# Kernel tuning notes

Hardware: AMD Instinct MI355X
Metric: run time of the kernel (lower is better)

## Reference

```python
import jax, jax.numpy as jnp
import numpy as np

V = 50257   # vocab size
E = 256     # embedding_dimension
D = 8       # key_query_reduced_dimensionality
H = 8       # no_of_attention_heads
L = 16      # no_of_blocks
B = 8       # batch
T = 512     # seq len == context_size
FF = 4 * E  # MLP hidden


def setup_inputs() -> dict:
    key = jax.random.key(0)
    ks = jax.random.split(key, 12)
    rn = lambda k, s: jax.random.normal(k, s, jnp.float32) * 0.02
    return {
        'tokens': jax.random.randint(ks[0], (B, T), 0, V),
        'ideal_value': jax.random.randint(ks[1], (B, T), 0, V),
        'tok_emb': rn(ks[2], (V, E)),
        'pos_emb': rn(ks[3], (T, E)),
        'Wq': rn(ks[4], (L, H, E, D)),
        'Wk': rn(ks[5], (L, H, E, D)),
        'Wv': rn(ks[6], (L, H, E, D)),
        'Wo': rn(ks[7], (L, H * D, E)),
        'bo': jnp.zeros((L, E), jnp.float32),
        'ln1_s': jnp.ones((L, E), jnp.float32),
        'ln1_b': jnp.zeros((L, E), jnp.float32),
        'W1': rn(ks[8], (L, E, FF)),
        'b1': jnp.zeros((L, FF), jnp.float32),
        'W2': rn(ks[9], (L, FF, E)),
        'b2': jnp.zeros((L, E), jnp.float32),
        'ln2_s': jnp.ones((L, E), jnp.float32),
        'ln2_b': jnp.zeros((L, E), jnp.float32),
        'lnf_s': jnp.ones((E,), jnp.float32),
        'lnf_b': jnp.zeros((E,), jnp.float32),
        'Wf': rn(ks[10], (E, V)),
        'bf': jnp.zeros((V,), jnp.float32),
    }


def _ln(x, s, b):
    m = x.mean(-1, keepdims=True)
    v = ((x - m) ** 2).mean(-1, keepdims=True)
    return (x - m) * jax.lax.rsqrt(v + 1e-5) * s + b


def reference(tokens, ideal_value, tok_emb, pos_emb, Wq, Wk, Wv, Wo, bo,
              ln1_s, ln1_b, W1, b1, W2, b2, ln2_s, ln2_b, lnf_s, lnf_b, Wf, bf):
    Bn, Tn = tokens.shape
    x = tok_emb[tokens] + pos_emb[:Tn]                      # [B,T,E]
    # faithful mask: masked_fill where transpose(tril(R))==0 -> keep upper triangle
    keep = jnp.triu(jnp.ones((D, D), bool))
    scale = jnp.float32(E) ** 0.5

    def block(x, p):
        wq, wk, wv, wo, bo_, s1, bb1, w1, bm1, w2, bm2, s2, bb2 = p
        h = _ln(x, s1, bb1)
        Q = jnp.einsum('bte,hed->bhtd', h, wq)              # [B,H,T,D]
        K = jnp.einsum('bte,hed->bhtd', h, wk)
        Vv = jnp.einsum('bte,hed->bhtd', h, wv)
        # R = K^T @ Q : feature-by-feature [B,H,D,D] (this repo's quirky attention)
        R = jnp.einsum('bhti,bhtj->bhij', K, Q) / scale
        R = jax.nn.softmax(jnp.where(keep, R, -jnp.inf), axis=-1)
        a = jnp.einsum('bhti,bhij->bhtj', Vv, R)            # V @ R, [B,H,T,D]
        a = a.transpose(0, 2, 1, 3).reshape(x.shape[0], x.shape[1], H * D)
        x = x + a @ wo + bo_                                # dropout is identity (eval)
        h2 = _ln(x, s2, bb2)
        x = x + jax.nn.relu(h2 @ w1 + bm1) @ w2 + bm2
        return x, None

    x, _ = jax.lax.scan(block, x, (Wq, Wk, Wv, Wo, bo, ln1_s, ln1_b,
                                   W1, b1, W2, b2, ln2_s, ln2_b))
    logits = (_ln(x, lnf_s, lnf_b) @ Wf + bf).reshape(-1, V)  # [B*T, V]
    tgt = ideal_value.reshape(-1)
    logp = jax.nn.log_softmax(logits, axis=-1)
    loss = -jnp.take_along_axis(logp, tgt[:, None], axis=1).mean()
    return logits, loss
```

## Files before the change

kernel.cpp:

```cpp
#include <hip/hip_runtime.h>
#include <math.h>

#define V_SZ 50257
#define NPAD 50432
#define NCB 197

#define AS1 __attribute__((address_space(1)))
#define AS3 __attribute__((address_space(3)))

typedef short s16x8 __attribute__((ext_vector_type(8)));
typedef ushort u16x4 __attribute__((ext_vector_type(4)));
typedef float f32x4 __attribute__((ext_vector_type(4)));

__device__ __forceinline__ ushort f2bf(float x) {
    union { float f; unsigned u; } v; v.f = x;
    unsigned r = v.u + 0x7FFF + ((v.u >> 16) & 1);
    return (ushort)(r >> 16);
}
__device__ __forceinline__ float bf2f(ushort u) {
    union { unsigned u; float f; } v; v.u = ((unsigned)u) << 16; return v.f;
}

__global__ __launch_bounds__(256) void gpt_embed_ln(const int* __restrict__ tokens,
                                                    const float* __restrict__ tok_emb,
                                                    const float* __restrict__ pos_emb,
                                                    const float* __restrict__ s, const float* __restrict__ b,
                                                    float* __restrict__ x, ushort* __restrict__ hb) {
    int wave = threadIdx.x >> 6, lane = threadIdx.x & 63;
    int row = blockIdx.x * 4 + wave;
    int t = row & 511;
    int tok = tokens[row];
    float4 te = ((const float4*)(tok_emb + tok * 256))[lane];
    float4 pe = ((const float4*)(pos_emb + t * 256))[lane];
    float4 v = make_float4(te.x + pe.x, te.y + pe.y, te.z + pe.z, te.w + pe.w);
    ((float4*)(x + row * 256))[lane] = v;
    float sum = v.x + v.y + v.z + v.w;
    #pragma unroll
    for (int off = 1; off < 64; off <<= 1) sum += __shfl_xor(sum, off);
    float mean = sum * (1.0f / 256.0f);
    float dx = v.x - mean, dy = v.y - mean, dz = v.z - mean, dw = v.w - mean;
    float vs = dx * dx + dy * dy + dz * dz + dw * dw;
    #pragma unroll
    for (int off = 1; off < 64; off <<= 1) vs += __shfl_xor(vs, off);
    float rstd = rsqrtf(vs * (1.0f / 256.0f) + 1e-5f);
    float4 sv = ((const float4*)s)[lane];
    float4 bv = ((const float4*)b)[lane];
    u16x4 o;
    o[0] = f2bf(dx * rstd * sv.x + bv.x);
    o[1] = f2bf(dy * rstd * sv.y + bv.y);
    o[2] = f2bf(dz * rstd * sv.z + bv.z);
    o[3] = f2bf(dw * rstd * sv.w + bv.w);
    *(u16x4*)&hb[row * 256 + lane * 4] = o;
}

__global__ __launch_bounds__(256) void cvt_transpose(const float* __restrict__ in, ushort* __restrict__ out,
                                                     int Kd, int Nd, int n_real,
                                                     int in_stride, int out_stride) {
    __shared__ __align__(16) ushort t[64][80];
    const float* inp = in + (size_t)blockIdx.z * in_stride;
    ushort* outp = out + (size_t)blockIdx.z * out_stride;
    int n0 = blockIdx.x * 64, k0 = blockIdx.y * 64;
    int tid = threadIdx.x;
    #pragma unroll
    for (int p = 0; p < 4; p++) {
        int lk = p * 16 + (tid >> 4);
        int ln = (tid & 15) * 4;
        int k = k0 + lk, n = n0 + ln;
        const float* rowp = inp + (size_t)k * Nd;
        float v0 = 0.f, v1 = 0.f, v2 = 0.f, v3 = 0.f;
        if (n + 0 < n_real) v0 = rowp[n + 0];
        if (n + 1 < n_real) v1 = rowp[n + 1];
        if (n + 2 < n_real) v2 = rowp[n + 2];
        if (n + 3 < n_real) v3 = rowp[n + 3];
        t[ln + 0][lk] = f2bf(v0);
        t[ln + 1][lk] = f2bf(v1);
        t[ln + 2][lk] = f2bf(v2);
        t[ln + 3][lk] = f2bf(v3);
    }
    __syncthreads();
    int ln = tid >> 2, kq = (tid & 3) * 16;
    ushort* op = outp + (size_t)(n0 + ln) * Kd + k0 + kq;
    *(s16x8*)&op[0] = *(const s16x8*)&t[ln][kq];
    *(s16x8*)&op[8] = *(const s16x8*)&t[ln][kq + 8];
}

__global__ __launch_bounds__(256) void cvt_qkv(const float* __restrict__ Wq, const float* __restrict__ Wk,
                                               const float* __restrict__ Wv, ushort* __restrict__ WqkvT) {
    int l = blockIdx.x, kind = blockIdx.y;
    const float* W = (kind == 0 ? Wq : (kind == 1 ? Wk : Wv)) + l * 16384;
    ushort* out = WqkvT + (size_t)l * 65536 + kind * 64 * 256;
    int tid = threadIdx.x;
    #pragma unroll 4
    for (int it = 0; it < 64; it++) {
        int idx = it * 256 + tid;
        int row = idx >> 8, e = idx & 255;
        int h = row >> 3, d = row & 7;
        out[row * 256 + e] = f2bf(W[h * 2048 + e * 8 + d]);
    }
    if (kind == 0) {
        ushort* zp = WqkvT + (size_t)l * 65536 + 192 * 256;
        #pragma unroll 4
        for (int it = 0; it < 64; it++) zp[it * 256 + tid] = 0;
    }
}

__global__ __launch_bounds__(512, 4) void gpt_pre(const ushort* __restrict__ hb,
                                                  const ushort* __restrict__ WqkvT,
                                                  ushort* __restrict__ Vb,
                                                  float* __restrict__ Rpart) {
    __shared__ __align__(16) ushort As[16 * 64];
    __shared__ __align__(16) ushort Bs[256 * 64];
    __shared__ float kqv[16][193];
    const int tid = threadIdx.x, lane = tid & 63, wn = tid >> 6;
    const int rows0 = blockIdx.x * 16;
    const int fr = lane & 15, fkb = (lane >> 4) * 16;
    const int arow = tid >> 3, ach = tid & 7;

    f32x4 acc[2];
    acc[0] = (f32x4)0.0f; acc[1] = (f32x4)0.0f;

    s16x8 ra, rb[4];
    if (tid < 128) ra = *(const s16x8*)&hb[(size_t)(rows0 + arow) * 256 + ach * 8];
    #pragma unroll
    for (int i = 0; i < 4; i++) {
        int u = tid + i * 512, r = u >> 3, ch = u & 7;
        rb[i] = *(const s16x8*)&WqkvT[(size_t)r * 256 + ch * 8];
    }
    #pragma unroll 1
    for (int kt = 0; kt < 4; kt++) {
        if (kt) __syncthreads();
        if (tid < 128)
            *(s16x8*)&As[arow * 64 + (((ach * 16) ^ ((arow & 7) << 4)) >> 1)] = ra;
        #pragma unroll
        for (int i = 0; i < 4; i++) {
            int u = tid + i * 512, r = u >> 3, ch = u & 7;
            *(s16x8*)&Bs[r * 64 + (((ch * 16) ^ ((r & 7) << 4)) >> 1)] = rb[i];
        }
        __syncthreads();
        if (kt < 3) {
            int k0 = (kt + 1) * 64;
            if (tid < 128) ra = *(const s16x8*)&hb[(size_t)(rows0 + arow) * 256 + k0 + ach * 8];
            #pragma unroll
            for (int i = 0; i < 4; i++) {
                int u = tid + i * 512, r = u >> 3, ch = u & 7;
                rb[i] = *(const s16x8*)&WqkvT[(size_t)r * 256 + k0 + ch * 8];
            }
        }
        #pragma unroll
        for (int kk = 0; kk < 2; kk++) {
            int kbyte = kk * 64 + fkb;
            s16x8 af = *(const s16x8*)&As[fr * 64 + ((kbyte ^ ((fr & 7) << 4)) >> 1)];
            #pragma unroll
            for (int n = 0; n < 2; n++) {
                int brow = wn * 32 + n * 16 + fr;
                s16x8 bfv = *(const s16x8*)&Bs[brow * 64 + ((kbyte ^ ((brow & 7) << 4)) >> 1)];
                acc[n] = __builtin_amdgcn_mfma_f32_16x16x32_bf16(af, bfv, acc[n], 0, 0, 0);
            }
        }
    }
    #pragma unroll
    for (int n = 0; n < 2; n++) {
        int col = wn * 32 + n * 16 + fr;
        if (col < 192) {
            #pragma unroll
            for (int r = 0; r < 4; r++)
                kqv[(lane >> 4) * 4 + r][col] = acc[n][r];
        }
    }
    __syncthreads();
    #pragma unroll
    for (int i = 0; i < 2; i++) {
        int u = tid + i * 512, t = u >> 6, hd = u & 63;
        Vb[(size_t)(rows0 + t) * 64 + hd] = f2bf(kqv[t][128 + hd]);
    }
    {
        int h = tid >> 6, i2 = (tid >> 3) & 7, j = tid & 7;
        float s = 0.0f;
        #pragma unroll
        for (int t = 0; t < 16; t++)
            s += kqv[t][64 + h * 8 + i2] * kqv[t][h * 8 + j];
        int bb = rows0 >> 9, part = (rows0 >> 4) & 31;
        Rpart[(size_t)(bb * 32 + part) * 512 + tid] = s;
    }
}

__global__ __launch_bounds__(512, 4) void gpt_layer(
        const float* __restrict__ Rpart_in, const ushort* __restrict__ Vb_in,
        const ushort* __restrict__ WoT, const float* __restrict__ bo,
        const ushort* __restrict__ W1T, const float* __restrict__ b1,
        const ushort* __restrict__ W2T, const float* __restrict__ b2,
        const float* __restrict__ ls2, const float* __restrict__ lb2,
        const float* __restrict__ nls, const float* __restrict__ nlb,
        float* __restrict__ x,
        const ushort* __restrict__ WqkvT_next,
        ushort* __restrict__ Vb_out, float* __restrict__ Rpart_out,
        ushort* __restrict__ hbout, int mode) {
    __shared__ __align__(16) ushort Bs[256 * 64];
    __shared__ __align__(16) ushort ffs[16 * 1024];
    __shared__ __align__(16) ushort h2s[16 * 256];
    __shared__ __align__(16) ushort abl[16 * 64];
    __shared__ __align__(16) ushort Vl[16 * 64];
    __shared__ float Rs[512];
    __shared__ float red1[16][8], red2[16][8], mrow[16], rrow[16];

    const int tid = threadIdx.x, lane = tid & 63, wn = tid >> 6;
    const int rows0 = blockIdx.x * 16, b = rows0 >> 9;
    const int fr = lane & 15, fkb = (lane >> 4) * 16, rbase = (lane >> 4) * 4;
    int colv[2]; colv[0] = wn * 32 + fr; colv[1] = wn * 32 + 16 + fr;

    {
        const float* rp = Rpart_in + (size_t)b * 32 * 512 + tid;
        float s = 0.0f;
        #pragma unroll
        for (int p = 0; p < 32; p++) s += rp[p * 512];
        s *= (1.0f / 16.0f);
        int ii = (tid >> 3) & 7, j = tid & 7;
        float val = (j >= ii) ? s : -INFINITY;
        float m = val;
        #pragma unroll
        for (int off = 1; off < 8; off <<= 1) m = fmaxf(m, __shfl_xor(m, off, 8));
        float ex = __expf(val - m);
        float su = ex;
        #pragma unroll
        for (int off = 1; off < 8; off <<= 1) su += __shfl_xor(su, off, 8);
        Rs[tid] = ex / su;
    }
    #pragma unroll
    for (int i = 0; i < 2; i++) {
        int u = tid + i * 512, t = u >> 6, hd = u & 63;
        Vl[t * 64 + hd] = Vb_in[(size_t)(rows0 + t) * 64 + hd];
    }
    __syncthreads();
    #pragma unroll
    for (int i = 0; i < 2; i++) {
        int u = tid + i * 512, t = u >> 6, hd = u & 63, h = hd >> 3, j = hd & 7;
        float a = 0.0f;
        #pragma unroll
        for (int q = 0; q < 8; q++)
            a += bf2f(Vl[t * 64 + h * 8 + q]) * Rs[h * 64 + q * 8 + j];
        abl[t * 64 + (((hd * 2) ^ ((t & 7) << 4)) >> 1)] = f2bf(a);
    }
    s16x8 rbv[4];
    #pragma unroll
    for (int i = 0; i < 4; i++) {
        int u = tid + i * 512, r = u >> 3, ch = u & 7;
        rbv[i] = *(const s16x8*)&WoT[(size_t)r * 64 + ch * 8];
    }
    __syncthreads();
    #pragma unroll
    for (int i = 0; i < 4; i++) {
        int u = tid + i * 512, r = u >> 3, ch = u & 7;
        *(s16x8*)&Bs[r * 64 + (((ch * 16) ^ ((r & 7) << 4)) >> 1)] = rbv[i];
    }
    __syncthreads();
    f32x4 acc[2];
    acc[0] = (f32x4)0.0f; acc[1] = (f32x4)0.0f;
    #pragma unroll
    for (int kk = 0; kk < 2; kk++) {
        int kbyte = kk * 64 + fkb;
        s16x8 af = *(const s16x8*)&abl[fr * 64 + ((kbyte ^ ((fr & 7) << 4)) >> 1)];
        #pragma unroll
        for (int n = 0; n < 2; n++) {
            int brow = wn * 32 + n * 16 + fr;
            s16x8 bfv = *(const s16x8*)&Bs[brow * 64 + ((kbyte ^ ((brow & 7) << 4)) >> 1)];
            acc[n] = __builtin_amdgcn_mfma_f32_16x16x32_bf16(af, bfv, acc[n], 0, 0, 0);
        }
    }
    float xn[2][4];
    #pragma unroll
    for (int n = 0; n < 2; n++) {
        int col = colv[n];
        float bbv = bo[col];
        #pragma unroll
        for (int r = 0; r < 4; r++)
            xn[n][r] = acc[n][r] + bbv + x[(size_t)(rows0 + rbase + r) * 256 + col];
    }
    #pragma unroll
    for (int r = 0; r < 4; r++) {
        float s1 = xn[0][r] + xn[1][r];
        float s2 = xn[0][r] * xn[0][r] + xn[1][r] * xn[1][r];
        #pragma unroll
        for (int off = 1; off < 16; off <<= 1) {
            s1 += __shfl_xor(s1, off);
            s2 += __shfl_xor(s2, off);
        }
        if (fr == 0) { red1[rbase + r][wn] = s1; red2[rbase + r][wn] = s2; }
    }
    __syncthreads();
    if (tid < 16) {
        float s1 = 0.f, s2 = 0.f;
        #pragma unroll
        for (int w = 0; w < 8; w++) { s1 += red1[tid][w]; s2 += red2[tid][w]; }
        float mean = s1 * (1.0f / 256.0f);
        float var = s2 * (1.0f / 256.0f) - mean * mean;
        mrow[tid] = mean;
        rrow[tid] = rsqrtf(var + 1e-5f);
    }
    __syncthreads();
    #pragma unroll
    for (int n = 0; n < 2; n++) {
        int col = colv[n];
        float lsv = ls2[col], lbv = lb2[col];
        #pragma unroll
        for (int r = 0; r < 4; r++) {
            int rl = rbase + r;
            float hv = (xn[n][r] - mrow[rl]) * rrow[rl] * lsv + lbv;
            h2s[rl * 256 + (((col * 2) ^ ((rl & 7) << 4)) >> 1)] = f2bf(hv);
        }
    }
    #pragma unroll 1
    for (int c = 0; c < 4; c++) {
        const ushort* Bg = W1T + (size_t)c * 256 * 256;
        acc[0] = (f32x4)0.0f; acc[1] = (f32x4)0.0f;
        #pragma unroll
        for (int i = 0; i < 4; i++) {
            int u = tid + i * 512, r = u >> 3, ch = u & 7;
            rbv[i] = *(const s16x8*)&Bg[(size_t)r * 256 + ch * 8];
        }
        #pragma unroll 1
        for (int kt = 0; kt < 4; kt++) {
            __syncthreads();
            #pragma unroll
            for (int i = 0; i < 4; i++) {
                int u = tid + i * 512, r = u >> 3, ch = u & 7;
                *(s16x8*)&Bs[r * 64 + (((ch * 16) ^ ((r & 7) << 4)) >> 1)] = rbv[i];
            }
            __syncthreads();
            if (kt < 3) {
                int k0 = (kt + 1) * 64;
                #pragma unroll
                for (int i = 0; i < 4; i++) {
                    int u = tid + i * 512, r = u >> 3, ch = u & 7;
                    rbv[i] = *(const s16x8*)&Bg[(size_t)r * 256 + k0 + ch * 8];
                }
            }
            #pragma unroll
            for (int kk = 0; kk < 2; kk++) {
                int kbyte = kt * 128 + kk * 64 + fkb;
                s16x8 af = *(const s16x8*)&h2s[fr * 256 + ((kbyte ^ ((fr & 7) << 4)) >> 1)];
                int kb2 = kk * 64 + fkb;
                #pragma unroll
                for (int n = 0; n < 2; n++) {
                    int brow = wn * 32 + n * 16 + fr;
                    s16x8 bfv = *(const s16x8*)&Bs[brow * 64 + ((kb2 ^ ((brow & 7) << 4)) >> 1)];
                    acc[n] = __builtin_amdgcn_mfma_f32_16x16x32_bf16(af, bfv, acc[n], 0, 0, 0);
                }
            }
        }
        #pragma unroll
        for (int n = 0; n < 2; n++) {
            int col = c * 256 + colv[n];
            float bb1 = b1[col];
            #pragma unroll
            for (int r = 0; r < 4; r++) {
                int rl = rbase + r;
                ffs[rl * 1024 + (((col * 2) ^ ((rl & 7) << 4)) >> 1)] =
                    f2bf(fmaxf(acc[n][r] + bb1, 0.0f));
            }
        }
    }
    f32x4 a2[2];
    a2[0] = (f32x4)0.0f; a2[1] = (f32x4)0.0f;
    #pragma unroll
    for (int i = 0; i < 4; i++) {
        int u = tid + i * 512, r = u >> 3, ch = u & 7;
        rbv[i] = *(const s16x8*)&W2T[(size_t)r * 1024 + ch * 8];
    }
    #pragma unroll 1
    for (int kt = 0; kt < 16; kt++) {
        __syncthreads();
        #pragma unroll
        for (int i = 0; i < 4; i++) {
            int u = tid + i * 512, r = u >> 3, ch = u & 7;
            *(s16x8*)&Bs[r * 64 + (((ch * 16) ^ ((r & 7) << 4)) >> 1)] = rbv[i];
        }
        __syncthreads();
        if (kt < 15) {
            int k0 = (kt + 1) * 64;
            #pragma unroll
            for (int i = 0; i < 4; i++) {
                int u = tid + i * 512, r = u >> 3, ch = u & 7;
                rbv[i] = *(const s16x8*)&W2T[(size_t)r * 1024 + k0 + ch * 8];
            }
        }
        #pragma unroll
        for (int kk = 0; kk < 2; kk++) {
            int kbyte = kt * 128 + kk * 64 + fkb;
            s16x8 af = *(const s16x8*)&ffs[fr * 1024 + ((kbyte ^ ((fr & 7) << 4)) >> 1)];
            int kb2 = kk * 64 + fkb;
            #pragma unroll
            for (int n = 0; n < 2; n++) {
                int brow = wn * 32 + n * 16 + fr;
                s16x8 bfv = *(const s16x8*)&Bs[brow * 64 + ((kb2 ^ ((brow & 7) << 4)) >> 1)];
                a2[n] = __builtin_amdgcn_mfma_f32_16x16x32_bf16(af, bfv, a2[n], 0, 0, 0);
            }
        }
    }
    #pragma unroll
    for (int n = 0; n < 2; n++) {
        int col = colv[n];
        float bb2 = b2[col];
        #pragma unroll
        for (int r = 0; r < 4; r++) {
            float v = xn[n][r] + a2[n][r] + bb2;
            xn[n][r] = v;
            x[(size_t)(rows0 + rbase + r) * 256 + col] = v;
        }
    }
    __syncthreads();
    #pragma unroll
    for (int r = 0; r < 4; r++) {
        float s1 = xn[0][r] + xn[1][r];
        float s2 = xn[0][r] * xn[0][r] + xn[1][r] * xn[1][r];
        #pragma unroll
        for (int off = 1; off < 16; off <<= 1) {
            s1 += __shfl_xor(s1, off);
            s2 += __shfl_xor(s2, off);
        }
        if (fr == 0) { red1[rbase + r][wn] = s1; red2[rbase + r][wn] = s2; }
    }
    __syncthreads();
    if (tid < 16) {
        float s1 = 0.f, s2 = 0.f;
        #pragma unroll
        for (int w = 0; w < 8; w++) { s1 += red1[tid][w]; s2 += red2[tid][w]; }
        float mean = s1 * (1.0f / 256.0f);
        float var = s2 * (1.0f / 256.0f) - mean * mean;
        mrow[tid] = mean;
        rrow[tid] = rsqrtf(var + 1e-5f);
    }
    __syncthreads();
    #pragma unroll
    for (int n = 0; n < 2; n++) {
        int col = colv[n];
        float lsv = nls[col], lbv = nlb[col];
        #pragma unroll
        for (int r = 0; r < 4; r++) {
            int rl = rbase + r;
            float hv = (xn[n][r] - mrow[rl]) * rrow[rl] * lsv + lbv;
            ushort hu = f2bf(hv);
            h2s[rl * 256 + (((col * 2) ^ ((rl & 7) << 4)) >> 1)] = hu;
            if (mode == 0)
                hbout[(size_t)(rows0 + rl) * 256 + col] = hu;
        }
    }
    if (mode == 0) return;

    float* kqv = (float*)ffs;
    acc[0] = (f32x4)0.0f; acc[1] = (f32x4)0.0f;
    #pragma unroll
    for (int i = 0; i < 4; i++) {
        int u = tid + i * 512, r = u >> 3, ch = u & 7;
        rbv[i] = *(const s16x8*)&WqkvT_next[(size_t)r * 256 + ch * 8];
    }
    #pragma unroll 1
    for (int kt = 0; kt < 4; kt++) {
        __syncthreads();
        #pragma unroll
        for (int i = 0; i < 4; i++) {
            int u = tid + i * 512, r = u >> 3, ch = u & 7;
            *(s16x8*)&Bs[r * 64 + (((ch * 16) ^ ((r & 7) << 4)) >> 1)] = rbv[i];
        }
        __syncthreads();
        if (kt < 3) {
            int k0 = (kt + 1) * 64;
            #pragma unroll
            for (int i = 0; i < 4; i++) {
                int u = tid + i * 512, r = u >> 3, ch = u & 7;
                rbv[i] = *(const s16x8*)&WqkvT_next[(size_t)r * 256 + k0 + ch * 8];
            }
        }
        #pragma unroll
        for (int kk = 0; kk < 2; kk++) {
            int kbyte = kt * 128 + kk * 64 + fkb;
            s16x8 af = *(const s16x8*)&h2s[fr * 256 + ((kbyte ^ ((fr & 7) << 4)) >> 1)];
            int kb2 = kk * 64 + fkb;
            #pragma unroll
            for (int n = 0; n < 2; n++) {
                int brow = wn * 32 + n * 16 + fr;
                s16x8 bfv = *(const s16x8*)&Bs[brow * 64 + ((kb2 ^ ((brow & 7) << 4)) >> 1)];
                acc[n] = __builtin_amdgcn_mfma_f32_16x16x32_bf16(af, bfv, acc[n], 0, 0, 0);
            }
        }
    }
    __syncthreads();
    #pragma unroll
    for (int n = 0; n < 2; n++) {
        int col = wn * 32 + n * 16 + fr;
        if (col < 192) {
            #pragma unroll
            for (int r = 0; r < 4; r++)
                kqv[(rbase + r) * 193 + col] = acc[n][r];
        }
    }
    __syncthreads();
    #pragma unroll
    for (int i = 0; i < 2; i++) {
        int u = tid + i * 512, t = u >> 6, hd = u & 63;
        Vb_out[(size_t)(rows0 + t) * 64 + hd] = f2bf(kqv[t * 193 + 128 + hd]);
    }
    {
        int h = tid >> 6, i2 = (tid >> 3) & 7, j = tid & 7;
        float s = 0.0f;
        #pragma unroll
        for (int t = 0; t < 16; t++)
            s += kqv[t * 193 + 64 + h * 8 + i2] * kqv[t * 193 + h * 8 + j];
        int part = (rows0 >> 4) & 31;
        Rpart_out[(size_t)(b * 32 + part) * 512 + tid] = s;
    }
}

__global__ __launch_bounds__(512, 4) void gpt_logits_mfma(const ushort* __restrict__ hb, const ushort* __restrict__ WfT,
                                                          const float* __restrict__ bfb, float* __restrict__ out,
                                                          float2* __restrict__ lsebuf) {
    __shared__ __align__(16) ushort As[128 * 64];
    __shared__ __align__(16) ushort Bs[256 * 64];
    f32x4 acc[4][4];
    int flat = blockIdx.y * 32 + blockIdx.x;
    int nf = (flat & 7) * 788 + (flat >> 3);
    int rb = nf & 31, cb = nf >> 5;
    int row0 = rb * 128, c0 = cb * 256;
    const int tid = threadIdx.x, lane = tid & 63, wid = tid >> 6;
    const int wm = wid >> 2, wn = wid & 3;
    const int fr = lane & 15, fkb = (lane >> 4) * 16;

    #pragma unroll
    for (int m = 0; m < 4; m++)
        #pragma unroll
        for (int n = 0; n < 4; n++) acc[m][n] = (f32x4)0.0f;

    const int srow = lane >> 3;
    const int sch = lane & 7;
    #pragma unroll 1
    for (int kt = 0; kt < 4; kt++) {
        if (kt) __syncthreads();
        {
            int kb = kt * 64;
            #pragma unroll
            for (int i = 0; i < 2; i++) {
                int rloc = wid * 16 + i * 8 + srow;
                int cs = sch ^ (rloc & 7);
                const ushort* gp = &hb[(size_t)(row0 + rloc) * 256 + kb + cs * 8];
                __builtin_amdgcn_global_load_lds((const AS1 void*)gp,
                                                 (AS3 void*)&As[(wid * 16 + i * 8) * 64], 16, 0, 0);
            }
            #pragma unroll
            for (int i = 0; i < 4; i++) {
                int rloc = wid * 32 + i * 8 + srow;
                int cs = sch ^ (rloc & 7);
                const ushort* gp = &WfT[(size_t)(c0 + rloc) * 256 + kb + cs * 8];
                __builtin_amdgcn_global_load_lds((const AS1 void*)gp,
                                                 (AS3 void*)&Bs[(wid * 32 + i * 8) * 64], 16, 0, 0);
            }
        }
        __syncthreads();
        #pragma unroll
        for (int kk = 0; kk < 2; kk++) {
            int kbyte = kk * 64 + fkb;
            s16x8 af[4], bfr[4];
            #pragma unroll
            for (int m = 0; m < 4; m++) {
                int arow = wm * 64 + m * 16 + fr;
                af[m] = *(const s16x8*)&As[arow * 64 + ((kbyte ^ ((arow & 7) << 4)) >> 1)];
            }
            #pragma unroll
            for (int n = 0; n < 4; n++) {
                int brow = wn * 64 + n * 16 + fr;
                bfr[n] = *(const s16x8*)&Bs[brow * 64 + ((kbyte ^ ((brow & 7) << 4)) >> 1)];
            }
            #pragma unroll
            for (int m = 0; m < 4; m++)
                #pragma unroll
                for (int n = 0; n < 4; n++)
                    acc[m][n] = __builtin_amdgcn_mfma_f32_16x16x32_bf16(af[m], bfr[n], acc[m][n], 0, 0, 0);
        }
    }
    float bb[4]; int gcv[4];
    #pragma unroll
    for (int n = 0; n < 4; n++) {
        int gc = c0 + wn * 64 + n * 16 + fr;
        gcv[n] = gc;
        bb[n] = (gc < V_SZ) ? bfb[gc] : 0.0f;
    }
    __syncthreads();
    float2 (*red)[4] = (float2(*)[4])As;
    #pragma unroll
    for (int m = 0; m < 4; m++) {
        int rloc = wm * 64 + m * 16 + (lane >> 4) * 4;
        int gr = row0 + rloc;
        #pragma unroll
        for (int r = 0; r < 4; r++) {
            float v[4];
            float vmax = -1e30f;
            #pragma unroll
            for (int n = 0; n < 4; n++) {
                v[n] = (gcv[n] < V_SZ) ? acc[m][n][r] + bb[n] : -1e30f;
                vmax = fmaxf(vmax, v[n]);
            }
            #pragma unroll
            for (int n = 0; n < 4; n++)
                if (gcv[n] < V_SZ)
                    out[(size_t)(gr + r) * V_SZ + gcv[n]] = v[n];
            #pragma unroll
            for (int off = 1; off < 16; off <<= 1)
                vmax = fmaxf(vmax, __shfl_xor(vmax, off));
            float vsum = __expf(v[0] - vmax) + __expf(v[1] - vmax)
                       + __expf(v[2] - vmax) + __expf(v[3] - vmax);
            #pragma unroll
            for (int off = 1; off < 16; off <<= 1)
                vsum += __shfl_xor(vsum, off);
            if ((lane & 15) == 0)
                red[rloc + r][wn] = make_float2(vmax, vsum);
        }
    }
    __syncthreads();
    if (tid < 128) {
        float M = -1e30f, S = 0.0f;
        #pragma unroll
        for (int w = 0; w < 4; w++) {
            float2 p = red[tid][w];
            float M2 = fmaxf(M, p.x);
            S = S * __expf(M - M2) + p.y * __expf(p.x - M2);
            M = M2;
        }
        lsebuf[(size_t)(row0 + tid) * NCB + cb] = make_float2(M, S);
    }
}

__global__ __launch_bounds__(256) void gpt_lse(const float2* __restrict__ lsebuf, const float* __restrict__ out,
                                               const int* __restrict__ tgt, float* __restrict__ partial) {
    int wave = threadIdx.x >> 6, lane = threadIdx.x & 63;
    int row = blockIdx.x * 4 + wave;
    float m = -INFINITY, s = 0.0f;
    for (int i = lane; i < NCB; i += 64) {
        float2 p = lsebuf[(size_t)row * NCB + i];
        float M = fmaxf(m, p.x);
        s = s * __expf(m - M) + p.y * __expf(p.x - M);
        m = M;
    }
    #pragma unroll
    for (int off = 1; off < 64; off <<= 1) {
        float m2 = __shfl_xor(m, off);
        float s2 = __shfl_xor(s, off);
        float M = fmaxf(m, m2);
        s = s * __expf(m - M) + s2 * __expf(m2 - M);
        m = M;
    }
    if (lane == 0)
        partial[row] = m + logf(s) - out[(size_t)row * V_SZ + tgt[row]];
}

__global__ void gpt_loss_reduce(const float* __restrict__ partial, float* __restrict__ out) {
    __shared__ float red[256];
    int tid = threadIdx.x;
    float s = 0.0f;
    for (int i = tid; i < 4096; i += 256) s += partial[i];
    red[tid] = s;
    __syncthreads();
    for (int off = 128; off > 0; off >>= 1) {
        if (tid < off) red[tid] += red[tid + off];
        __syncthreads();
    }
    if (tid == 0) out[0] = red[0] * (1.0f / 4096.0f);
}

__global__ void gpt_embed(const int* __restrict__ tokens, const float* __restrict__ tok_emb,
                          const float* __restrict__ pos_emb, float* __restrict__ x) {
    int idx = blockIdx.x * 256 + threadIdx.x;
    int bt = idx >> 8, e = idx & 255;
    int t = bt & 511;
    int tok = tokens[bt];
    x[idx] = tok_emb[tok * 256 + e] + pos_emb[t * 256 + e];
}

__global__ void gpt_ln(const float* __restrict__ x, const float* __restrict__ s,
                       const float* __restrict__ b, float* __restrict__ h) {
    __shared__ float red[256];
    int row = blockIdx.x, e = threadIdx.x;
    float v = x[row * 256 + e];
    red[e] = v;
    __syncthreads();
    for (int off = 128; off > 0; off >>= 1) {
        if (e < off) red[e] += red[e + off];
        __syncthreads();
    }
    float mean = red[0] * (1.0f / 256.0f);
    __syncthreads();
    float d = v - mean;
    red[e] = d * d;
    __syncthreads();
    for (int off = 128; off > 0; off >>= 1) {
        if (e < off) red[e] += red[e + off];
        __syncthreads();
    }
    float rstd = rsqrtf(red[0] * (1.0f / 256.0f) + 1e-5f);
    h[row * 256 + e] = d * rstd * s[e] + b[e];
}

__global__ void gpt_qkv(const float* __restrict__ h, const float* __restrict__ Wq,
                        const float* __restrict__ Wk, const float* __restrict__ Wv,
                        float* __restrict__ Q, float* __restrict__ K, float* __restrict__ Vv) {
    __shared__ float hs[8][256];
    int tid = threadIdx.x;
    int row0 = blockIdx.x * 8;
    #pragma unroll
    for (int r = 0; r < 8; r++) hs[r][tid] = h[(row0 + r) * 256 + tid];
    __syncthreads();
    if (tid < 192) {
        int kind = tid >> 6, o = tid & 63, hh = o >> 3, d = o & 7;
        const float* W = kind == 0 ? Wq : (kind == 1 ? Wk : Wv);
        const float* wp = W + hh * 2048 + d;
        float acc[8];
        #pragma unroll
        for (int r = 0; r < 8; r++) acc[r] = 0.0f;
        for (int e = 0; e < 256; e++) {
            float w = wp[e * 8];
            #pragma unroll
            for (int r = 0; r < 8; r++) acc[r] += hs[r][e] * w;
        }
        float* outp = kind == 0 ? Q : (kind == 1 ? K : Vv);
        int b = row0 >> 9;
        #pragma unroll
        for (int r = 0; r < 8; r++) {
            int t = (row0 + r) & 511;
            outp[((b * 8 + hh) * 512 + t) * 8 + d] = acc[r];
        }
    }
}

__global__ void gpt_attn_r(const float* __restrict__ K, const float* __restrict__ Q,
                           float* __restrict__ R) {
    __shared__ __align__(16) float Ks[64][8];
    __shared__ __align__(16) float Qs[64][8];
    int bh = blockIdx.x, tid = threadIdx.x;
    int i = tid >> 3, j = tid & 7;
    const float* Kb = K + bh * 512 * 8;
    const float* Qb = Q + bh * 512 * 8;
    float acc = 0.0f;
    for (int t0 = 0; t0 < 512; t0 += 64) {
        *(float4*)&Ks[tid][0] = *(const float4*)&Kb[(t0 + tid) * 8];
        *(float4*)&Ks[tid][4] = *(const float4*)&Kb[(t0 + tid) * 8 + 4];
        *(float4*)&Qs[tid][0] = *(const float4*)&Qb[(t0 + tid) * 8];
        *(float4*)&Qs[tid][4] = *(const float4*)&Qb[(t0 + tid) * 8 + 4];
        __syncthreads();
        #pragma unroll 16
        for (int t = 0; t < 64; t++) acc += Ks[t][i] * Qs[t][j];
        __syncthreads();
    }
    acc *= (1.0f / 16.0f);
    float val = (j >= i) ? acc : -INFINITY;
    float m = val;
    #pragma unroll
    for (int off = 1; off < 8; off <<= 1) m = fmaxf(m, __shfl_xor(m, off, 8));
    float ex = expf(val - m);
    float sum = ex;
    #pragma unroll
    for (int off = 1; off < 8; off <<= 1) sum += __shfl_xor(sum, off, 8);
    R[bh * 64 + tid] = ex / sum;
}

__global__ void gpt_attn_out(const float* __restrict__ Vv, const float* __restrict__ R,
                             const float* __restrict__ Wo, const float* __restrict__ bo,
                             float* __restrict__ x) {
    __shared__ __align__(16) float as[8][64];
    int tid = threadIdx.x;
    int row0 = blockIdx.x * 8;
    int b = row0 >> 9;
    #pragma unroll
    for (int k = 0; k < 2; k++) {
        int idx = k * 256 + tid;
        int r = idx >> 6, hd = idx & 63;
        int hh = hd >> 3, jj = hd & 7;
        int t = (row0 + r) & 511;
        const float* vp = Vv + ((b * 8 + hh) * 512 + t) * 8;
        const float* rp = R + (b * 8 + hh) * 64 + jj;
        float a = 0.0f;
        #pragma unroll
        for (int i = 0; i < 8; i++) a += vp[i] * rp[i * 8];
        as[r][hd] = a;
    }
    __syncthreads();
    float acc[8];
    float bb = bo[tid];
    #pragma unroll
    for (int r = 0; r < 8; r++) acc[r] = bb;
    for (int hd0 = 0; hd0 < 64; hd0 += 4) {
        float w0 = Wo[(hd0 + 0) * 256 + tid];
        float w1 = Wo[(hd0 + 1) * 256 + tid];
        float w2 = Wo[(hd0 + 2) * 256 + tid];
        float w3 = Wo[(hd0 + 3) * 256 + tid];
        #pragma unroll
        for (int r = 0; r < 8; r++) {
            float4 av = *(const float4*)&as[r][hd0];
            acc[r] += av.x * w0 + av.y * w1 + av.z * w2 + av.w * w3;
        }
    }
    #pragma unroll
    for (int r = 0; r < 8; r++) x[(row0 + r) * 256 + tid] += acc[r];
}

__global__ __launch_bounds__(256) void gpt_mlp(const float* __restrict__ h, const float* __restrict__ W1,
                         const float* __restrict__ b1, const float* __restrict__ W2,
                         const float* __restrict__ b2, float* __restrict__ x) {
    __shared__ __align__(16) float hs[8][256];
    __shared__ __align__(16) float ffs[8][1024];
    int tid = threadIdx.x;
    int row0 = blockIdx.x * 8;
    #pragma unroll
    for (int r = 0; r < 8; r++) hs[r][tid] = h[(row0 + r) * 256 + tid];
    __syncthreads();
    {
        float acc[4][8];
        #pragma unroll
        for (int k = 0; k < 4; k++) {
            float bb = b1[k * 256 + tid];
            #pragma unroll
            for (int r = 0; r < 8; r++) acc[k][r] = bb;
        }
        for (int e0 = 0; e0 < 256; e0 += 4) {
            float w[4][4];
            #pragma unroll
            for (int ee = 0; ee < 4; ee++)
                #pragma unroll
                for (int k = 0; k < 4; k++)
                    w[ee][k] = W1[(e0 + ee) * 1024 + k * 256 + tid];
            #pragma unroll
            for (int r = 0; r < 8; r++) {
                float4 hv = *(const float4*)&hs[r][e0];
                #pragma unroll
                for (int k = 0; k < 4; k++)
                    acc[k][r] += hv.x * w[0][k] + hv.y * w[1][k] + hv.z * w[2][k] + hv.w * w[3][k];
            }
        }
        #pragma unroll
        for (int k = 0; k < 4; k++)
            #pragma unroll
            for (int r = 0; r < 8; r++)
                ffs[r][k * 256 + tid] = fmaxf(acc[k][r], 0.0f);
    }
    __syncthreads();
    {
        float acc[8];
        float bb = b2[tid];
        #pragma unroll
        for (int r = 0; r < 8; r++) acc[r] = bb;
        for (int f0 = 0; f0 < 1024; f0 += 4) {
            float w0 = W2[(f0 + 0) * 256 + tid];
            float w1 = W2[(f0 + 1) * 256 + tid];
            float w2 = W2[(f0 + 2) * 256 + tid];
            float w3 = W2[(f0 + 3) * 256 + tid];
            #pragma unroll
            for (int r = 0; r < 8; r++) {
                float4 fv = *(const float4*)&ffs[r][f0];
                acc[r] += fv.x * w0 + fv.y * w1 + fv.z * w2 + fv.w * w3;
            }
        }
        #pragma unroll
        for (int r = 0; r < 8; r++) x[(row0 + r) * 256 + tid] += acc[r];
    }
}

__global__ __launch_bounds__(256) void gpt_logits(const float* __restrict__ hf, const float* __restrict__ Wf,
                            const float* __restrict__ bf, float* __restrict__ out) {
    __shared__ __align__(16) float hs[32][256];
    int tid = threadIdx.x;
    int row0 = blockIdx.y * 32;
    #pragma unroll
    for (int r = 0; r < 32; r++) hs[r][tid] = hf[(row0 + r) * 256 + tid];
    __syncthreads();
    int c0 = blockIdx.x * 512 + tid;
    int c1 = c0 + 256;
    int c0c = c0 < V_SZ ? c0 : V_SZ - 1;
    int c1c = c1 < V_SZ ? c1 : V_SZ - 1;
    float acc0[32], acc1[32];
    float b0 = bf[c0c], b1 = bf[c1c];
    #pragma unroll
    for (int r = 0; r < 32; r++) { acc0[r] = b0; acc1[r] = b1; }
    const float* p0 = Wf + c0c;
    const float* p1 = Wf + c1c;
    for (int e0 = 0; e0 < 256; e0 += 4) {
        float w00 = p0[(size_t)(e0 + 0) * V_SZ];
        float w01 = p0[(size_t)(e0 + 1) * V_SZ];
        float w02 = p0[(size_t)(e0 + 2) * V_SZ];
        float w03 = p0[(size_t)(e0 + 3) * V_SZ];
        float w10 = p1[(size_t)(e0 + 0) * V_SZ];
        float w11 = p1[(size_t)(e0 + 1) * V_SZ];
        float w12 = p1[(size_t)(e0 + 2) * V_SZ];
        float w13 = p1[(size_t)(e0 + 3) * V_SZ];
        #pragma unroll
        for (int r = 0; r < 32; r++) {
            float4 hv = *(const float4*)&hs[r][e0];
            acc0[r] += hv.x * w00 + hv.y * w01 + hv.z * w02 + hv.w * w03;
            acc1[r] += hv.x * w10 + hv.y * w11 + hv.z * w12 + hv.w * w13;
        }
    }
    if (c0 < V_SZ) {
        #pragma unroll
        for (int r = 0; r < 32; r++) out[(size_t)(row0 + r) * V_SZ + c0] = acc0[r];
    }
    if (c1 < V_SZ) {
        #pragma unroll
        for (int r = 0; r < 32; r++) out[(size_t)(row0 + r) * V_SZ + c1] = acc1[r];
    }
}

__global__ void gpt_loss(const float* __restrict__ logits, const int* __restrict__ tgt,
                         float* __restrict__ partial) {
    __shared__ float ms[256], ss[256];
    int row = blockIdx.x, tid = threadIdx.x;
    const float* lr = logits + (size_t)row * V_SZ;
    float m = -INFINITY, s = 0.0f;
    for (int c = tid; c < V_SZ; c += 256) {
        float v = lr[c];
        float nm = fmaxf(m, v);
        s = s * expf(m - nm) + expf(v - nm);
        m = nm;
    }
    ms[tid] = m; ss[tid] = s;
    __syncthreads();
    for (int off = 128; off > 0; off >>= 1) {
        if (tid < off) {
            float m2 = ms[tid + off], s2 = ss[tid + off];
            float M = fmaxf(ms[tid], m2);
            ss[tid] = ss[tid] * expf(ms[tid] - M) + s2 * expf(m2 - M);
            ms[tid] = M;
        }
        __syncthreads();
    }
    if (tid == 0) {
        float lse = ms[0] + logf(ss[0]);
        partial[row] = lse - lr[tgt[row]];
    }
}

extern "C" void kernel_launch(void* const* d_in, const int* in_sizes, int n_in,
                              void* d_out, int out_size, void* d_ws, size_t ws_size,
                              hipStream_t stream) {
    const int*   tokens  = (const int*)d_in[0];
    const int*   ideal   = (const int*)d_in[1];
    const float* tok_emb = (const float*)d_in[2];
    const float* pos_emb = (const float*)d_in[3];
    const float* Wq      = (const float*)d_in[4];
    const float* Wk      = (const float*)d_in[5];
    const float* Wv      = (const float*)d_in[6];
    const float* Wo      = (const float*)d_in[7];
    const float* bo      = (const float*)d_in[8];
    const float* ln1_s   = (const float*)d_in[9];
    const float* ln1_b   = (const float*)d_in[10];
    const float* W1      = (const float*)d_in[11];
    const float* b1      = (const float*)d_in[12];
    const float* W2      = (const float*)d_in[13];
    const float* b2      = (const float*)d_in[14];
    const float* ln2_s   = (const float*)d_in[15];
    const float* ln2_b   = (const float*)d_in[16];
    const float* lnf_s   = (const float*)d_in[17];
    const float* lnf_b   = (const float*)d_in[18];
    const float* Wf      = (const float*)d_in[19];
    const float* bf      = (const float*)d_in[20];
    float* out = (float*)d_out;

    size_t off = 0;
    char* wsc = (char*)d_ws;
    ushort* WfT   = (ushort*)(wsc + off); off += (size_t)NPAD * 256 * 2;
    ushort* W1T   = (ushort*)(wsc + off); off += (size_t)16 * 1024 * 256 * 2;
    ushort* W2T   = (ushort*)(wsc + off); off += (size_t)16 * 256 * 1024 * 2;
    ushort* WqkvT = (ushort*)(wsc + off); off += (size_t)16 * 256 * 256 * 2;
    ushort* WoT   = (ushort*)(wsc + off); off += (size_t)16 * 256 * 64 * 2;
    ushort* hb    = (ushort*)(wsc + off); off += (size_t)4096 * 256 * 2;
    ushort* Vb0   = (ushort*)(wsc + off); off += (size_t)4096 * 64 * 2;
    ushort* Vb1   = (ushort*)(wsc + off); off += (size_t)4096 * 64 * 2;
    float*  x     = (float*)(wsc + off);  off += (size_t)4096 * 256 * 4;
    float*  Rp0   = (float*)(wsc + off);  off += (size_t)8 * 32 * 512 * 4;
    float*  Rp1   = (float*)(wsc + off);  off += (size_t)8 * 32 * 512 * 4;
    float*  partial = (float*)(wsc + off); off += (size_t)4096 * 4;
    float2* lsebuf = (float2*)(wsc + off); off += (size_t)4096 * NCB * 8;
    bool big = ws_size >= off;

    if (big) {
        cvt_transpose<<<dim3(16, 4, 16), 256, 0, stream>>>(W1, W1T, 256, 1024, 1024, 262144, 262144);
        cvt_transpose<<<dim3(4, 16, 16), 256, 0, stream>>>(W2, W2T, 1024, 256, 256, 262144, 262144);
        cvt_transpose<<<dim3(4, 1, 16), 256, 0, stream>>>(Wo, WoT, 64, 256, 256, 16384, 16384);
        cvt_transpose<<<dim3(788, 4, 1), 256, 0, stream>>>(Wf, WfT, 256, V_SZ, V_SZ, 0, 0);
        cvt_qkv<<<dim3(16, 3), 256, 0, stream>>>(Wq, Wk, Wv, WqkvT);

        gpt_embed_ln<<<1024, 256, 0, stream>>>(tokens, tok_emb, pos_emb, ln1_s, ln1_b, x, hb);
        gpt_pre<<<256, 512, 0, stream>>>(hb, WqkvT, Vb0, Rp0);

        for (int l = 0; l < 16; l++) {
            const float* nls = (l < 15) ? ln1_s + (l + 1) * 256 : lnf_s;
            const float* nlb = (l < 15) ? ln1_b + (l + 1) * 256 : lnf_b;
            const float* Rin = (l & 1) ? Rp1 : Rp0;
            const ushort* Vin = (l & 1) ? Vb1 : Vb0;
            float* Rout = (l & 1) ? Rp0 : Rp1;
            ushort* Vout = (l & 1) ? Vb0 : Vb1;
            int mode = (l < 15) ? 1 : 0;
            const ushort* Wnext = WqkvT + (size_t)((l < 15) ? (l + 1) : 0) * 65536;
            gpt_layer<<<256, 512, 0, stream>>>(Rin, Vin,
                                               WoT + (size_t)l * 16384, bo + l * 256,
                                               W1T + (size_t)l * 262144, b1 + l * 1024,
                                               W2T + (size_t)l * 262144, b2 + l * 256,
                                               ln2_s + l * 256, ln2_b + l * 256,
                                               nls, nlb, x,
                                               Wnext, Vout, Rout, hb, mode);
        }

        gpt_logits_mfma<<<dim3(32, NCB), 512, 0, stream>>>(hb, WfT, bf, out, lsebuf);
        gpt_lse<<<1024, 256, 0, stream>>>(lsebuf, out, ideal, partial);
        gpt_loss_reduce<<<1, 256, 0, stream>>>(partial, out + (size_t)4096 * V_SZ);
    } else {
        float* fx  = (float*)d_ws;
        float* fh  = fx + 4096 * 256;
        float* fQ  = fh + 4096 * 256;
        float* fK  = fQ + 4096 * 64;
        float* fV  = fK + 4096 * 64;
        float* fR  = fV + 4096 * 64;
        float* fpart = fR + 64 * 64;
        gpt_embed<<<4096, 256, 0, stream>>>(tokens, tok_emb, pos_emb, fx);
        for (int l = 0; l < 16; l++) {
            gpt_ln<<<4096, 256, 0, stream>>>(fx, ln1_s + l * 256, ln1_b + l * 256, fh);
            gpt_qkv<<<512, 256, 0, stream>>>(fh, Wq + l * 16384, Wk + l * 16384, Wv + l * 16384, fQ, fK, fV);
            gpt_attn_r<<<64, 64, 0, stream>>>(fK, fQ, fR);
            gpt_attn_out<<<512, 256, 0, stream>>>(fV, fR, Wo + l * 16384, bo + l * 256, fx);
            gpt_ln<<<4096, 256, 0, stream>>>(fx, ln2_s + l * 256, ln2_b + l * 256, fh);
            gpt_mlp<<<512, 256, 0, stream>>>(fh, W1 + l * 262144, b1 + l * 1024, W2 + l * 262144, b2 + l * 256, fx);
        }
        gpt_ln<<<4096, 256, 0, stream>>>(fx, lnf_s, lnf_b, fh);
        dim3 lg(99, 128);
        gpt_logits<<<lg, 256, 0, stream>>>(fh, Wf, bf, out);
        gpt_loss<<<4096, 256, 0, stream>>>(out, ideal, fpart);
        gpt_loss_reduce<<<1, 256, 0, stream>>>(fpart, out + (size_t)4096 * V_SZ);
    }
}
```

Baseline: 1.005 ms.

## Make B-tile LDS staging wave-private to drop per-k-step block barriers

Each wave now stages into shared memory only the 32 weight rows it consumes in its MFMAs, instead of all 512 threads cooperatively filling the whole 256-row tile. Because no other wave reads those rows, the two __syncthreads around every k-step in the Wo, W1, W2 and next-layer QKV loops are removed. A single barrier is kept at each phase boundary so the shared activation buffers (h2s, ffs) are visible to all waves. This relies on in-order LDS access within a wave and adds a small unroll of the W2 loop; the trade is less overlap of load latency across waves at barriers in exchange for removing barrier stalls.

```diff
diff --git a/kernel.cpp b/kernel.cpp
--- a/kernel.cpp
+++ b/kernel.cpp
@@ -207,6 +207,13 @@
     const int rows0 = blockIdx.x * 16, b = rows0 >> 9;
     const int fr = lane & 15, fkb = (lane >> 4) * 16, rbase = (lane >> 4) * 4;
     int colv[2]; colv[0] = wn * 32 + fr; colv[1] = wn * 32 + 16 + fr;
+    int srow_[4], sch_[4];
+    #pragma unroll
+    for (int i = 0; i < 4; i++) {
+        int u = lane + i * 64;
+        srow_[i] = wn * 32 + (u >> 3);
+        sch_[i] = u & 7;
+    }
 
     {
         const float* rp = Rpart_in + (size_t)b * 32 * 512 + tid;
@@ -242,17 +249,12 @@
     }
     s16x8 rbv[4];
     #pragma unroll
-    for (int i = 0; i < 4; i++) {
-        int u = tid + i * 512, r = u >> 3, ch = u & 7;
-        rbv[i] = *(const s16x8*)&WoT[(size_t)r * 64 + ch * 8];
-    }
-    __syncthreads();
-    #pragma unroll
-    for (int i = 0; i < 4; i++) {
-        int u = tid + i * 512, r = u >> 3, ch = u & 7;
-        *(s16x8*)&Bs[r * 64 + (((ch * 16) ^ ((r & 7) << 4)) >> 1)] = rbv[i];
-    }
-    __syncthreads();
+    for (int i = 0; i < 4; i++)
+        rbv[i] = *(const s16x8*)&WoT[(size_t)srow_[i] * 64 + sch_[i] * 8];
+    __syncthreads();
+    #pragma unroll
+    for (int i = 0; i < 4; i++)
+        *(s16x8*)&Bs[srow_[i] * 64 + (((sch_[i] * 16) ^ ((srow_[i] & 7) << 4)) >> 1)] = rbv[i];
     f32x4 acc[2];
     acc[0] = (f32x4)0.0f; acc[1] = (f32x4)0.0f;
     #pragma unroll
@@ -308,31 +310,24 @@
             h2s[rl * 256 + (((col * 2) ^ ((rl & 7) << 4)) >> 1)] = f2bf(hv);
         }
     }
+    __syncthreads();
     #pragma unroll 1
     for (int c = 0; c < 4; c++) {
         const ushort* Bg = W1T + (size_t)c * 256 * 256;
         acc[0] = (f32x4)0.0f; acc[1] = (f32x4)0.0f;
         #pragma unroll
-        for (int i = 0; i < 4; i++) {
-            int u = tid + i * 512, r = u >> 3, ch = u & 7;
-            rbv[i] = *(const s16x8*)&Bg[(size_t)r * 256 + ch * 8];
-        }
+        for (int i = 0; i < 4; i++)
+            rbv[i] = *(const s16x8*)&Bg[(size_t)srow_[i] * 256 + sch_[i] * 8];
         #pragma unroll 1
         for (int kt = 0; kt < 4; kt++) {
-            __syncthreads();
-            #pragma unroll
-            for (int i = 0; i < 4; i++) {
-                int u = tid + i * 512, r = u >> 3, ch = u & 7;
-                *(s16x8*)&Bs[r * 64 + (((ch * 16) ^ ((r & 7) << 4)) >> 1)] = rbv[i];
-            }
-            __syncthreads();
+            #pragma unroll
+            for (int i = 0; i < 4; i++)
+                *(s16x8*)&Bs[srow_[i] * 64 + (((sch_[i] * 16) ^ ((srow_[i] & 7) << 4)) >> 1)] = rbv[i];
             if (kt < 3) {
                 int k0 = (kt + 1) * 64;
                 #pragma unroll
-                for (int i = 0; i < 4; i++) {
-                    int u = tid + i * 512, r = u >> 3, ch = u & 7;
-                    rbv[i] = *(const s16x8*)&Bg[(size_t)r * 256 + k0 + ch * 8];
-                }
+                for (int i = 0; i < 4; i++)
+                    rbv[i] = *(const s16x8*)&Bg[(size_t)srow_[i] * 256 + k0 + sch_[i] * 8];
             }
             #pragma unroll
             for (int kk = 0; kk < 2; kk++) {
@@ -359,29 +354,22 @@
             }
         }
     }
+    __syncthreads();
     f32x4 a2[2];
     a2[0] = (f32x4)0.0f; a2[1] = (f32x4)0.0f;
     #pragma unroll
-    for (int i = 0; i < 4; i++) {
-        int u = tid + i * 512, r = u >> 3, ch = u & 7;
-        rbv[i] = *(const s16x8*)&W2T[(size_t)r * 1024 + ch * 8];
-    }
-    #pragma unroll 1
+    for (int i = 0; i < 4; i++)
+        rbv[i] = *(const s16x8*)&W2T[(size_t)srow_[i] * 1024 + sch_[i] * 8];
+    #pragma unroll 2
     for (int kt = 0; kt < 16; kt++) {
-        __syncthreads();
-        #pragma unroll
-        for (int i = 0; i < 4; i++) {
-            int u = tid + i * 512, r = u >> 3, ch = u & 7;
-            *(s16x8*)&Bs[r * 64 + (((ch * 16) ^ ((r & 7) << 4)) >> 1)] = rbv[i];
-        }
-        __syncthreads();
+        #pragma unroll
+        for (int i = 0; i < 4; i++)
+            *(s16x8*)&Bs[srow_[i] * 64 + (((sch_[i] * 16) ^ ((srow_[i] & 7) << 4)) >> 1)] = rbv[i];
         if (kt < 15) {
             int k0 = (kt + 1) * 64;
             #pragma unroll
-            for (int i = 0; i < 4; i++) {
-                int u = tid + i * 512, r = u >> 3, ch = u & 7;
-                rbv[i] = *(const s16x8*)&W2T[(size_t)r * 1024 + k0 + ch * 8];
-            }
+            for (int i = 0; i < 4; i++)
+                rbv[i] = *(const s16x8*)&W2T[(size_t)srow_[i] * 1024 + k0 + sch_[i] * 8];
         }
         #pragma unroll
         for (int kk = 0; kk < 2; kk++) {
@@ -445,30 +433,23 @@
         }
     }
     if (mode == 0) return;
+    __syncthreads();
 
     float* kqv = (float*)ffs;
     acc[0] = (f32x4)0.0f; acc[1] = (f32x4)0.0f;
     #pragma unroll
-    for (int i = 0; i < 4; i++) {
-        int u = tid + i * 512, r = u >> 3, ch = u & 7;
-        rbv[i] = *(const s16x8*)&WqkvT_next[(size_t)r * 256 + ch * 8];
-    }
+    for (int i = 0; i < 4; i++)
+        rbv[i] = *(const s16x8*)&WqkvT_next[(size_t)srow_[i] * 256 + sch_[i] * 8];
     #pragma unroll 1
     for (int kt = 0; kt < 4; kt++) {
-        __syncthreads();
-        #pragma unroll
-        for (int i = 0; i < 4; i++) {
-            int u = tid + i * 512, r = u >> 3, ch = u & 7;
-            *(s16x8*)&Bs[r * 64 + (((ch * 16) ^ ((r & 7) << 4)) >> 1)] = rbv[i];
-        }
-        __syncthreads();
+        #pragma unroll
+        for (int i = 0; i < 4; i++)
+            *(s16x8*)&Bs[srow_[i] * 64 + (((sch_[i] * 16) ^ ((srow_[i] & 7) << 4)) >> 1)] = rbv[i];
         if (kt < 3) {
             int k0 = (kt + 1) * 64;
             #pragma unroll
-            for (int i = 0; i < 4; i++) {
-                int u = tid + i * 512, r = u >> 3, ch = u & 7;
-                rbv[i] = *(const s16x8*)&WqkvT_next[(size_t)r * 256 + k0 + ch * 8];
-            }
+            for (int i = 0; i < 4; i++)
+                rbv[i] = *(const s16x8*)&WqkvT_next[(size_t)srow_[i] * 256 + k0 + sch_[i] * 8];
         }
         #pragma unroll
         for (int kk = 0; kk < 2; kk++) {
```

Result: faster. 917.2 us (-8.7%).
